# Kernel tuning notes

Hardware: AMD Instinct MI355X
Metric: run time of the kernel (lower is better)

The kernel has to match this reference:

```python
import jax, jax.numpy as jnp
import numpy as np

EPS = 1e-10
TAU = 1.0


def setup_inputs() -> dict:
    key = jax.random.key(0)
    ks = jax.random.split(key, 5)
    n, d = 1024, 64
    h1, h2, out = 128, 64, 2
    X = jax.random.normal(ks[0], (n, d), dtype=jnp.float32)
    W1 = jax.random.normal(ks[1], (2 * d, h1), dtype=jnp.float32) * (1.0 / np.sqrt(2 * d))
    b1 = jnp.zeros((h1,), dtype=jnp.float32)
    W2 = jax.random.normal(ks[2], (h1, h2), dtype=jnp.float32) * (1.0 / np.sqrt(h1))
    b2 = jnp.zeros((h2,), dtype=jnp.float32)
    W3 = jax.random.normal(ks[3], (h2, out), dtype=jnp.float32) * (1.0 / np.sqrt(h2))
    b3 = jnp.zeros((out,), dtype=jnp.float32)
    u = jax.random.uniform(ks[4], (n, n, out), dtype=jnp.float32)
    return {"X": X, "W1": W1, "b1": b1, "W2": W2, "b2": b2, "W3": W3, "b3": b3, "u": u}


def _mlp(h, W1, b1, W2, b2, W3, b3):
    h = jax.nn.relu(h @ W1 + b1)
    h = jax.nn.relu(h @ W2 + b2)
    return h @ W3 + b3


def reference(X, W1, b1, W2, b2, W3, b3, u):
    n, d = X.shape
    # pairwise features: pair[i, j] = concat(x_i, x_j)  -> (n, n, 2d)
    pair = jnp.concatenate(
        [jnp.broadcast_to(X[:, None, :], (n, n, d)),
         jnp.broadcast_to(X[None, :, :], (n, n, d))], axis=-1)
    logits = _mlp(pair, W1, b1, W2, b2, W3, b3)  # (n, n, 2)
    # undirected: mlp(pair.permute(1,0,2))[i,j] == mlp(pair)[j,i] (row-wise MLP)
    logits = 0.5 * (logits + jnp.swapaxes(logits, 0, 1))
    # gumbel-softmax, hard=True (straight-through)
    g = -jnp.log(-jnp.log(u + EPS) + EPS)
    y_soft = jax.nn.softmax((logits + g) / TAU, axis=-1)
    y_hard = jax.nn.one_hot(jnp.argmax(y_soft, axis=-1), y_soft.shape[-1], dtype=y_soft.dtype)
    y = jax.lax.stop_gradient(y_hard - y_soft) + y_soft
    # narrow(dim=2, start=1, size=1).squeeze() -> adjacency (n, n)
    return y[..., 1]
```

## Files before the change

kernel.cpp:

```cpp
#include <hip/hip_runtime.h>
#include <hip/hip_bf16.h>

#define N 1024
#define D 64
#define H1 128
#define H2 64
#define FLAG_THRESH 0.015f
#define FLAG_CAP 1024
#define H1PAD 136

typedef _Float16 half8 __attribute__((ext_vector_type(8)));
typedef float float4v __attribute__((ext_vector_type(4)));

__global__ __launch_bounds__(128) void precompute_kernel(
    const float* __restrict__ X, const float* __restrict__ W1,
    const float* __restrict__ b1,
    double* __restrict__ A64, double* __restrict__ B64,
    _Float16* __restrict__ A16, _Float16* __restrict__ B16)
{
    int i = blockIdx.x;
    int k = threadIdx.x;
    double a = (double)b1[k];
    double b = 0.0;
    for (int c = 0; c < D; ++c) {
        double x = (double)X[i * D + c];
        a += x * (double)W1[c * H1 + k];
        b += x * (double)W1[(D + c) * H1 + k];
    }
    A64[i * H1 + k] = a;
    B64[i * H1 + k] = b;
    A16[i * H1 + k] = (_Float16)(float)a;
    B16[i * H1 + k] = (_Float16)(float)b;
}

__global__ __launch_bounds__(256, 2) void fused_pair_kernel(
    const _Float16* __restrict__ A16, const _Float16* __restrict__ B16,
    const double* __restrict__ A64, const double* __restrict__ B64,
    const float* __restrict__ W2, const float* __restrict__ b2,
    const float* __restrict__ W3, const float* __restrict__ b3,
    const float* __restrict__ u, float* __restrict__ out)
{
    __shared__ _Float16 Ar[64 * H1PAD];
    __shared__ _Float16 Br[64 * H1PAD];
    __shared__ _Float16 W2t[64 * H1PAD];
    __shared__ __align__(16) unsigned char overlay[2 * 32 * 33 * 4];
    __shared__ unsigned int lflags[FLAG_CAP];
    __shared__ unsigned int lcnt;

    float (*Sij)[33] = (float(*)[33])overlay;
    float (*Sji)[33] = (float(*)[33])(overlay + 32 * 33 * 4);

    int tid = threadIdx.x;
    int t = blockIdx.x, ti = 0;
    while (t >= 32 - ti) { t -= 32 - ti; ++ti; }
    int tj = ti + t;
    int I0 = ti << 5, J0 = tj << 5;
    if (tid == 0) lcnt = 0;

    #pragma unroll
    for (int it = 0; it < 4; ++it) {
        int v = tid + it * 256;
        int row = v >> 4;
        int col = (v & 15) << 3;
        int gr = (row < 32) ? (I0 + row) : (J0 + row - 32);
        *(half8*)&Ar[row * H1PAD + col] = *(const half8*)&A16[(size_t)gr * H1 + col];
        *(half8*)&Br[row * H1PAD + col] = *(const half8*)&B16[(size_t)gr * H1 + col];
    }
    #pragma unroll
    for (int r = 0; r < 32; ++r) {
        int idx = tid + r * 256;
        int k = idx >> 6, n = idx & 63;
        W2t[n * H1PAD + k] = (_Float16)W2[idx];
    }
    __syncthreads();

    int lane = tid & 63;
    int wave = tid >> 6;
    int quad = lane >> 4;
    int m = lane & 15;

    half8 afrag[4][4];
    #pragma unroll
    for (int ks = 0; ks < 4; ++ks)
        #pragma unroll
        for (int nt = 0; nt < 4; ++nt)
            afrag[ks][nt] = *(const half8*)&W2t[(m + 16 * nt) * H1PAD + quad * 8 + 32 * ks];

    float b2x[4][4], w3x[4][4];
    #pragma unroll
    for (int nt = 0; nt < 4; ++nt)
        #pragma unroll
        for (int reg = 0; reg < 4; ++reg) {
            int o = (quad << 2) + reg + (nt << 4);
            b2x[nt][reg] = b2[o];
            w3x[nt][reg] = W3[o * 2 + 1] - W3[o * 2 + 0];
        }

    const half8 zero8 = {0, 0, 0, 0, 0, 0, 0, 0};

    int dir = wave >> 1;
    int jh = wave & 1;
    int abase = dir ? 32 : 0;
    int bbase = dir ? 0 : 32;
    float (*Sout)[33] = dir ? Sji : Sij;

    half8 hb[4];
    #pragma unroll
    for (int ks = 0; ks < 4; ++ks)
        hb[ks] = *(const half8*)&Br[(bbase + jh * 16 + m) * H1PAD + quad * 8 + 32 * ks];

    #pragma unroll 1
    for (int ii = 0; ii < 32; ++ii) {
        float4v acc[4];
        #pragma unroll
        for (int nt = 0; nt < 4; ++nt)
            acc[nt] = (float4v){b2x[nt][0], b2x[nt][1], b2x[nt][2], b2x[nt][3]};

        #pragma unroll
        for (int ks = 0; ks < 4; ++ks) {
            half8 ha = *(const half8*)&Ar[(abase + ii) * H1PAD + quad * 8 + 32 * ks];
            half8 h = __builtin_elementwise_max(ha + hb[ks], zero8);
            #pragma unroll
            for (int nt = 0; nt < 4; ++nt)
                acc[nt] = __builtin_amdgcn_mfma_f32_16x16x32_f16(afrag[ks][nt], h, acc[nt], 0, 0, 0);
        }
        float s = 0.f;
        #pragma unroll
        for (int nt = 0; nt < 4; ++nt)
            #pragma unroll
            for (int reg = 0; reg < 4; ++reg)
                s = fmaf(fmaxf(acc[nt][reg], 0.f), w3x[nt][reg], s);
        s += __shfl_xor(s, 16, 64);
        s += __shfl_xor(s, 32, 64);
        if (quad == 0) Sout[ii][jh * 16 + m] = s;
    }
    __syncthreads();

    float b3d = b3[1] - b3[0];
    {
        int i = tid >> 3, j0 = (tid & 7) << 2;
        int ij0 = (I0 + i) * N + (J0 + j0);
        float4 u01 = *(const float4*)&u[((size_t)ij0) * 2];
        float4 u23 = *(const float4*)&u[((size_t)ij0) * 2 + 4];
        float uu[8] = {u01.x, u01.y, u01.z, u01.w, u23.x, u23.y, u23.z, u23.w};
        float4 res; float* resp = &res.x;
        #pragma unroll
        for (int q = 0; q < 4; ++q) {
            int j = j0 + q;
            float l0 = -__logf(uu[2 * q] + 1e-10f) + 1e-10f;
            float l1 = -__logf(uu[2 * q + 1] + 1e-10f) + 1e-10f;
            float Dv = 0.5f * (Sij[i][j] + Sji[j][i]) + b3d + __logf(l0 / l1);
            resp[q] = Dv > 0.f ? 1.f : 0.f;
            if (fabsf(Dv) < FLAG_THRESH) {
                unsigned int idx = atomicAdd(&lcnt, 1u);
                if (idx < FLAG_CAP) lflags[idx] = (unsigned int)(ij0 + q);
            }
        }
        *(float4*)&out[ij0] = res;
    }
    if (ti != tj) {
        int j = tid >> 3, i0 = (tid & 7) << 2;
        int ij0 = (J0 + j) * N + (I0 + i0);
        float4 u01 = *(const float4*)&u[((size_t)ij0) * 2];
        float4 u23 = *(const float4*)&u[((size_t)ij0) * 2 + 4];
        float uu[8] = {u01.x, u01.y, u01.z, u01.w, u23.x, u23.y, u23.z, u23.w};
        float4 res; float* resp = &res.x;
        #pragma unroll
        for (int q = 0; q < 4; ++q) {
            int i = i0 + q;
            float l0 = -__logf(uu[2 * q] + 1e-10f) + 1e-10f;
            float l1 = -__logf(uu[2 * q + 1] + 1e-10f) + 1e-10f;
            float Dv = 0.5f * (Sji[j][i] + Sij[i][j]) + b3d + __logf(l0 / l1);
            resp[q] = Dv > 0.f ? 1.f : 0.f;
            if (fabsf(Dv) < FLAG_THRESH) {
                unsigned int idx = atomicAdd(&lcnt, 1u);
                if (idx < FLAG_CAP) lflags[idx] = (unsigned int)(ij0 + q);
            }
        }
        *(float4*)&out[ij0] = res;
    }

    __syncthreads();

    unsigned int nl = lcnt;
    if (nl > FLAG_CAP) nl = FLAG_CAP;
    double (*h1s)[2][H1] = (double(*)[2][H1])overlay;
    double w3dd = (double)W3[lane * 2 + 1] - (double)W3[lane * 2 + 0];
    double b2d = (double)b2[lane];

    for (unsigned int f = wave; f < nl; f += 4) {
        int ij = (int)lflags[f];
        int i = ij >> 10, j = ij & (N - 1);
        double uvd = 0.0;
        if (lane < 2) uvd = (double)u[(((size_t)ij) << 1) + lane];
        {
            int k0 = lane, k1 = lane + 64;
            double ai0 = A64[(size_t)i * H1 + k0], ai1 = A64[(size_t)i * H1 + k1];
            double aj0 = A64[(size_t)j * H1 + k0], aj1 = A64[(size_t)j * H1 + k1];
            double bi0 = B64[(size_t)i * H1 + k0], bi1 = B64[(size_t)i * H1 + k1];
            double bj0 = B64[(size_t)j * H1 + k0], bj1 = B64[(size_t)j * H1 + k1];
            double v;
            v = ai0 + bj0; h1s[wave][0][k0] = v > 0.0 ? v : 0.0;
            v = ai1 + bj1; h1s[wave][0][k1] = v > 0.0 ? v : 0.0;
            v = aj0 + bi0; h1s[wave][1][k0] = v > 0.0 ? v : 0.0;
            v = aj1 + bi1; h1s[wave][1][k1] = v > 0.0 ? v : 0.0;
        }
        asm volatile("s_waitcnt lgkmcnt(0)" ::: "memory");
        __builtin_amdgcn_wave_barrier();

        const double* __restrict__ hap = h1s[wave][0];
        const double* __restrict__ hbp = h1s[wave][1];
        double sa0 = 0.0, sa1 = 0.0, sa2 = 0.0, sa3 = 0.0;
        double sb0 = 0.0, sb1 = 0.0, sb2 = 0.0, sb3 = 0.0;
        #pragma unroll 2
        for (int k = 0; k < H1; k += 4) {
            double w0 = (double)W2[(k + 0) * H2 + lane];
            double w1 = (double)W2[(k + 1) * H2 + lane];
            double w2v = (double)W2[(k + 2) * H2 + lane];
            double w3v = (double)W2[(k + 3) * H2 + lane];
            sa0 += hap[k + 0] * w0;  sa1 += hap[k + 1] * w1;
            sa2 += hap[k + 2] * w2v; sa3 += hap[k + 3] * w3v;
            sb0 += hbp[k + 0] * w0;  sb1 += hbp[k + 1] * w1;
            sb2 += hbp[k + 2] * w2v; sb3 += hbp[k + 3] * w3v;
        }
        double sa = ((sa0 + sa1) + (sa2 + sa3)) + b2d;
        double sb = ((sb0 + sb1) + (sb2 + sb3)) + b2d;
        if (sa < 0.0) sa = 0.0;
        if (sb < 0.0) sb = 0.0;
        double da = sa * w3dd;
        double db = sb * w3dd;
        #pragma unroll
        for (int off = 32; off > 0; off >>= 1) {
            da += __shfl_down(da, off, 64);
            db += __shfl_down(db, off, 64);
        }
        double g = 0.0;
        if (lane < 2) g = -log(-log(uvd + 1e-10) + 1e-10);
        double g0 = __shfl(g, 0, 64);
        double g1 = __shfl(g, 1, 64);
        if (lane == 0) {
            double b3dd = (double)b3[1] - (double)b3[0];
            double Dv = 0.5 * (da + db) + b3dd + (g1 - g0);
            out[ij] = Dv > 0.0 ? 1.f : 0.f;
        }
        __builtin_amdgcn_wave_barrier();
    }
}

extern "C" void kernel_launch(void* const* d_in, const int* in_sizes, int n_in,
                              void* d_out, int out_size, void* d_ws, size_t ws_size,
                              hipStream_t stream) {
    const float* X  = (const float*)d_in[0];
    const float* W1 = (const float*)d_in[1];
    const float* b1 = (const float*)d_in[2];
    const float* W2 = (const float*)d_in[3];
    const float* b2 = (const float*)d_in[4];
    const float* W3 = (const float*)d_in[5];
    const float* b3 = (const float*)d_in[6];
    const float* u  = (const float*)d_in[7];
    float* out = (float*)d_out;

    double* A64 = (double*)d_ws;
    double* B64 = A64 + (size_t)N * H1;
    _Float16* A16 = (_Float16*)(B64 + (size_t)N * H1);
    _Float16* B16 = A16 + (size_t)N * H1;

    precompute_kernel<<<N, 128, 0, stream>>>(X, W1, b1, A64, B64, A16, B16);
    fused_pair_kernel<<<528, 256, 0, stream>>>(A16, B16, A64, B64,
                                               W2, b2, W3, b3, u, out);
}
```

Before: 151.8 us.

## Shrink pair tiles to 16x16, precompute transposed fp16 W2 in global memory

The fused pair kernel moves from 32x32 to 16x16 upper-triangular tiles, so the grid grows from 528 to 2080 blocks. The W2 transpose and fp16 conversion now happen once in the precompute kernel, and each block loads its MFMA A-fragments directly from global memory. This removes the per-block shared-memory W2 transpose and cuts LDS use, which allows 3 blocks per CU, and the u loads are issued early before the MLP work. In exchange, each block reuses less of its loaded rows, per-block fixed costs (fragment loads, biases) are repeated across 4x more blocks, and the lower flag cap could overflow if many pairs fall near the decision threshold.

```diff
diff --git a/kernel.cpp b/kernel.cpp
--- a/kernel.cpp
+++ b/kernel.cpp
@@ -6,7 +6,7 @@
 #define H1 128
 #define H2 64
 #define FLAG_THRESH 0.015f
-#define FLAG_CAP 1024
+#define FLAG_CAP 256
 #define H1PAD 136
 
 typedef _Float16 half8 __attribute__((ext_vector_type(8)));
@@ -14,10 +14,19 @@
 
 __global__ __launch_bounds__(128) void precompute_kernel(
     const float* __restrict__ X, const float* __restrict__ W1,
-    const float* __restrict__ b1,
+    const float* __restrict__ b1, const float* __restrict__ W2,
     double* __restrict__ A64, double* __restrict__ B64,
-    _Float16* __restrict__ A16, _Float16* __restrict__ B16)
+    _Float16* __restrict__ A16, _Float16* __restrict__ B16,
+    _Float16* __restrict__ W2T)
 {
+    if (blockIdx.x < 8) {
+        #pragma unroll
+        for (int e = 0; e < 8; ++e) {
+            int idx = blockIdx.x * 1024 + threadIdx.x * 8 + e;
+            int n = idx >> 7, k = idx & 127;
+            W2T[idx] = (_Float16)W2[k * H2 + n];
+        }
+    }
     int i = blockIdx.x;
     int k = threadIdx.x;
     double a = (double)b1[k];
@@ -33,46 +42,43 @@
     B16[i * H1 + k] = (_Float16)(float)b;
 }
 
-__global__ __launch_bounds__(256, 2) void fused_pair_kernel(
+__global__ __launch_bounds__(256, 3) void fused_pair_kernel(
     const _Float16* __restrict__ A16, const _Float16* __restrict__ B16,
+    const _Float16* __restrict__ W2T,
     const double* __restrict__ A64, const double* __restrict__ B64,
     const float* __restrict__ W2, const float* __restrict__ b2,
     const float* __restrict__ W3, const float* __restrict__ b3,
     const float* __restrict__ u, float* __restrict__ out)
 {
-    __shared__ _Float16 Ar[64 * H1PAD];
-    __shared__ _Float16 Br[64 * H1PAD];
-    __shared__ _Float16 W2t[64 * H1PAD];
-    __shared__ __align__(16) unsigned char overlay[2 * 32 * 33 * 4];
+    __shared__ __align__(16) _Float16 Ar[32 * H1PAD];
+    __shared__ __align__(16) _Float16 Br[32 * H1PAD];
+    __shared__ float Sij[16][17];
+    __shared__ float Sji[16][17];
     __shared__ unsigned int lflags[FLAG_CAP];
     __shared__ unsigned int lcnt;
 
-    float (*Sij)[33] = (float(*)[33])overlay;
-    float (*Sji)[33] = (float(*)[33])(overlay + 32 * 33 * 4);
-
     int tid = threadIdx.x;
     int t = blockIdx.x, ti = 0;
-    while (t >= 32 - ti) { t -= 32 - ti; ++ti; }
+    while (t >= 64 - ti) { t -= 64 - ti; ++ti; }
     int tj = ti + t;
-    int I0 = ti << 5, J0 = tj << 5;
+    int I0 = ti << 4, J0 = tj << 4;
     if (tid == 0) lcnt = 0;
 
-    #pragma unroll
-    for (int it = 0; it < 4; ++it) {
-        int v = tid + it * 256;
+    int i1 = tid >> 4, j1 = tid & 15;
+    int ijA = (I0 + i1) * N + (J0 + j1);
+    int ijB = (J0 + i1) * N + (I0 + j1);
+    float2 uA = *(const float2*)&u[((size_t)ijA) * 2];
+    float2 uB = *(const float2*)&u[((size_t)ijB) * 2];
+
+    #pragma unroll
+    for (int itr = 0; itr < 2; ++itr) {
+        int v = tid + itr * 256;
         int row = v >> 4;
         int col = (v & 15) << 3;
-        int gr = (row < 32) ? (I0 + row) : (J0 + row - 32);
+        int gr = (row < 16) ? (I0 + row) : (J0 + row - 16);
         *(half8*)&Ar[row * H1PAD + col] = *(const half8*)&A16[(size_t)gr * H1 + col];
         *(half8*)&Br[row * H1PAD + col] = *(const half8*)&B16[(size_t)gr * H1 + col];
     }
-    #pragma unroll
-    for (int r = 0; r < 32; ++r) {
-        int idx = tid + r * 256;
-        int k = idx >> 6, n = idx & 63;
-        W2t[n * H1PAD + k] = (_Float16)W2[idx];
-    }
-    __syncthreads();
 
     int lane = tid & 63;
     int wave = tid >> 6;
@@ -84,7 +90,7 @@
     for (int ks = 0; ks < 4; ++ks)
         #pragma unroll
         for (int nt = 0; nt < 4; ++nt)
-            afrag[ks][nt] = *(const half8*)&W2t[(m + 16 * nt) * H1PAD + quad * 8 + 32 * ks];
+            afrag[ks][nt] = *(const half8*)&W2T[(m + 16 * nt) * H1 + quad * 8 + 32 * ks];
 
     float b2x[4][4], w3x[4][4];
     #pragma unroll
@@ -95,22 +101,24 @@
             b2x[nt][reg] = b2[o];
             w3x[nt][reg] = W3[o * 2 + 1] - W3[o * 2 + 0];
         }
+    __syncthreads();
 
     const half8 zero8 = {0, 0, 0, 0, 0, 0, 0, 0};
 
     int dir = wave >> 1;
-    int jh = wave & 1;
-    int abase = dir ? 32 : 0;
-    int bbase = dir ? 0 : 32;
-    float (*Sout)[33] = dir ? Sji : Sij;
+    int ih = wave & 1;
+    int abase = dir ? 16 : 0;
+    int bbase = dir ? 0 : 16;
+    float (*Sout)[17] = dir ? Sji : Sij;
 
     half8 hb[4];
     #pragma unroll
     for (int ks = 0; ks < 4; ++ks)
-        hb[ks] = *(const half8*)&Br[(bbase + jh * 16 + m) * H1PAD + quad * 8 + 32 * ks];
+        hb[ks] = *(const half8*)&Br[(bbase + m) * H1PAD + quad * 8 + 32 * ks];
 
     #pragma unroll 1
-    for (int ii = 0; ii < 32; ++ii) {
+    for (int r = 0; r < 8; ++r) {
+        int row = ih * 8 + r;
         float4v acc[4];
         #pragma unroll
         for (int nt = 0; nt < 4; ++nt)
@@ -118,7 +126,7 @@
 
         #pragma unroll
         for (int ks = 0; ks < 4; ++ks) {
-            half8 ha = *(const half8*)&Ar[(abase + ii) * H1PAD + quad * 8 + 32 * ks];
+            half8 ha = *(const half8*)&Ar[(abase + row) * H1PAD + quad * 8 + 32 * ks];
             half8 h = __builtin_elementwise_max(ha + hb[ks], zero8);
             #pragma unroll
             for (int nt = 0; nt < 4; ++nt)
@@ -132,73 +140,51 @@
                 s = fmaf(fmaxf(acc[nt][reg], 0.f), w3x[nt][reg], s);
         s += __shfl_xor(s, 16, 64);
         s += __shfl_xor(s, 32, 64);
-        if (quad == 0) Sout[ii][jh * 16 + m] = s;
+        if (quad == 0) Sout[row][m] = s;
     }
     __syncthreads();
 
     float b3d = b3[1] - b3[0];
     {
-        int i = tid >> 3, j0 = (tid & 7) << 2;
-        int ij0 = (I0 + i) * N + (J0 + j0);
-        float4 u01 = *(const float4*)&u[((size_t)ij0) * 2];
-        float4 u23 = *(const float4*)&u[((size_t)ij0) * 2 + 4];
-        float uu[8] = {u01.x, u01.y, u01.z, u01.w, u23.x, u23.y, u23.z, u23.w};
-        float4 res; float* resp = &res.x;
-        #pragma unroll
-        for (int q = 0; q < 4; ++q) {
-            int j = j0 + q;
-            float l0 = -__logf(uu[2 * q] + 1e-10f) + 1e-10f;
-            float l1 = -__logf(uu[2 * q + 1] + 1e-10f) + 1e-10f;
-            float Dv = 0.5f * (Sij[i][j] + Sji[j][i]) + b3d + __logf(l0 / l1);
-            resp[q] = Dv > 0.f ? 1.f : 0.f;
-            if (fabsf(Dv) < FLAG_THRESH) {
-                unsigned int idx = atomicAdd(&lcnt, 1u);
-                if (idx < FLAG_CAP) lflags[idx] = (unsigned int)(ij0 + q);
-            }
-        }
-        *(float4*)&out[ij0] = res;
+        float l0 = -__logf(uA.x + 1e-10f) + 1e-10f;
+        float l1 = -__logf(uA.y + 1e-10f) + 1e-10f;
+        float Dv = 0.5f * (Sij[i1][j1] + Sji[j1][i1]) + b3d + __logf(l0 / l1);
+        out[ijA] = Dv > 0.f ? 1.f : 0.f;
+        if (fabsf(Dv) < FLAG_THRESH) {
+            unsigned int idx = atomicAdd(&lcnt, 1u);
+            if (idx < FLAG_CAP) lflags[idx] = (unsigned int)ijA;
+        }
     }
     if (ti != tj) {
-        int j = tid >> 3, i0 = (tid & 7) << 2;
-        int ij0 = (J0 + j) * N + (I0 + i0);
-        float4 u01 = *(const float4*)&u[((size_t)ij0) * 2];
-        float4 u23 = *(const float4*)&u[((size_t)ij0) * 2 + 4];
-        float uu[8] = {u01.x, u01.y, u01.z, u01.w, u23.x, u23.y, u23.z, u23.w};
-        float4 res; float* resp = &res.x;
-        #pragma unroll
-        for (int q = 0; q < 4; ++q) {
-            int i = i0 + q;
-            float l0 = -__logf(uu[2 * q] + 1e-10f) + 1e-10f;
-            float l1 = -__logf(uu[2 * q + 1] + 1e-10f) + 1e-10f;
-            float Dv = 0.5f * (Sji[j][i] + Sij[i][j]) + b3d + __logf(l0 / l1);
-            resp[q] = Dv > 0.f ? 1.f : 0.f;
-            if (fabsf(Dv) < FLAG_THRESH) {
-                unsigned int idx = atomicAdd(&lcnt, 1u);
-                if (idx < FLAG_CAP) lflags[idx] = (unsigned int)(ij0 + q);
-            }
-        }
-        *(float4*)&out[ij0] = res;
+        float l0 = -__logf(uB.x + 1e-10f) + 1e-10f;
+        float l1 = -__logf(uB.y + 1e-10f) + 1e-10f;
+        float Dv = 0.5f * (Sji[i1][j1] + Sij[j1][i1]) + b3d + __logf(l0 / l1);
+        out[ijB] = Dv > 0.f ? 1.f : 0.f;
+        if (fabsf(Dv) < FLAG_THRESH) {
+            unsigned int idx = atomicAdd(&lcnt, 1u);
+            if (idx < FLAG_CAP) lflags[idx] = (unsigned int)ijB;
+        }
     }
 
     __syncthreads();
 
     unsigned int nl = lcnt;
     if (nl > FLAG_CAP) nl = FLAG_CAP;
-    double (*h1s)[2][H1] = (double(*)[2][H1])overlay;
+    double (*h1s)[2][H1] = (double(*)[2][H1])Ar;
     double w3dd = (double)W3[lane * 2 + 1] - (double)W3[lane * 2 + 0];
     double b2d = (double)b2[lane];
 
     for (unsigned int f = wave; f < nl; f += 4) {
         int ij = (int)lflags[f];
-        int i = ij >> 10, j = ij & (N - 1);
+        int ii = ij >> 10, jj = ij & (N - 1);
         double uvd = 0.0;
         if (lane < 2) uvd = (double)u[(((size_t)ij) << 1) + lane];
         {
             int k0 = lane, k1 = lane + 64;
-            double ai0 = A64[(size_t)i * H1 + k0], ai1 = A64[(size_t)i * H1 + k1];
-            double aj0 = A64[(size_t)j * H1 + k0], aj1 = A64[(size_t)j * H1 + k1];
-            double bi0 = B64[(size_t)i * H1 + k0], bi1 = B64[(size_t)i * H1 + k1];
-            double bj0 = B64[(size_t)j * H1 + k0], bj1 = B64[(size_t)j * H1 + k1];
+            double ai0 = A64[(size_t)ii * H1 + k0], ai1 = A64[(size_t)ii * H1 + k1];
+            double aj0 = A64[(size_t)jj * H1 + k0], aj1 = A64[(size_t)jj * H1 + k1];
+            double bi0 = B64[(size_t)ii * H1 + k0], bi1 = B64[(size_t)ii * H1 + k1];
+            double bj0 = B64[(size_t)jj * H1 + k0], bj1 = B64[(size_t)jj * H1 + k1];
             double v;
             v = ai0 + bj0; h1s[wave][0][k0] = v > 0.0 ? v : 0.0;
             v = ai1 + bj1; h1s[wave][0][k1] = v > 0.0 ? v : 0.0;
@@ -264,8 +250,9 @@
     double* B64 = A64 + (size_t)N * H1;
     _Float16* A16 = (_Float16*)(B64 + (size_t)N * H1);
     _Float16* B16 = A16 + (size_t)N * H1;
-
-    precompute_kernel<<<N, 128, 0, stream>>>(X, W1, b1, A64, B64, A16, B16);
-    fused_pair_kernel<<<528, 256, 0, stream>>>(A16, B16, A64, B64,
-                                               W2, b2, W3, b3, u, out);
+    _Float16* W2T = B16 + (size_t)N * H1;
+
+    precompute_kernel<<<N, 128, 0, stream>>>(X, W1, b1, W2, A64, B64, A16, B16, W2T);
+    fused_pair_kernel<<<2080, 256, 0, stream>>>(A16, B16, W2T, A64, B64,
+                                                W2, b2, W3, b3, u, out);
 }
```

After: 136.9 us. 1.11x faster.
